# Kernel optimization log

Hardware: AMD Instinct MI355X
Metric: run time of the kernel (lower is better)

Reference implementation:

```python
import jax, jax.numpy as jnp
import numpy as np

T = 8192
C = 768
HEAD = 64

def setup_inputs() -> dict:
    key = jax.random.key(0)
    k0, k1, k2, k3 = jax.random.split(key, 4)
    tokens = jax.random.normal(k0, (T, C), dtype=jnp.float32)
    Wk = jax.random.normal(k1, (C, HEAD), dtype=jnp.float32) * (1.0 / np.sqrt(C))
    Wq = jax.random.normal(k2, (C, HEAD), dtype=jnp.float32) * (1.0 / np.sqrt(C))
    Wv = jax.random.normal(k3, (C, HEAD), dtype=jnp.float32) * (1.0 / np.sqrt(C))
    return {"tokens": tokens, "Wk": Wk, "Wq": Wq, "Wv": Wv}

def reference(tokens, Wk, Wq, Wv):
    # Single-head causal attention, faithful to source (scale = C**0.5, a multiply).
    keys = tokens @ Wk          # [T, H]
    queries = tokens @ Wq       # [T, H]
    values = tokens @ Wv        # [T, H]
    c = tokens.shape[-1]
    wei = (queries @ keys.T) * (c ** 0.5)                 # [T, T]
    causal = jnp.tril(jnp.ones((tokens.shape[0], tokens.shape[0]), dtype=bool))
    wei = jnp.where(causal, wei, -jnp.inf)
    wei = jax.nn.softmax(wei, axis=-1)
    return wei @ values         # [T, H]; dropout inactive (training=False)
```

## Files before the change

### kernel.cpp

```cpp
#include <hip/hip_runtime.h>
#include <math.h>

#define T_TOK 8192
#define C_DIM 768
#define H_DIM 64
#define SCALE_LOG2E (27.712812921102035f * 1.4426950408889634f)
#define NSPLIT 4

typedef _Float16 half8 __attribute__((ext_vector_type(8)));
typedef float floatx4 __attribute__((ext_vector_type(4)));

#define MFMA16(a, b, c) __builtin_amdgcn_mfma_f32_16x16x32_f16(a, b, c, 0, 0, 0)
#define WAIT_LGKM0() __builtin_amdgcn_s_waitcnt(0xC07F)
#define EXP2F(x) __builtin_amdgcn_exp2f(x)

typedef __attribute__((address_space(3))) void lds_void;
typedef const __attribute__((address_space(1))) void gbl_void;
#define GLOAD16(gp, lp) \
    __builtin_amdgcn_global_load_lds((gbl_void*)(gp), (lds_void*)(lp), 16, 0, 0)

template <int K> struct IC { static constexpr int v = K; };


__global__ __launch_bounds__(64) void wconvert_kernel(
    const float* __restrict__ Wk, const float* __restrict__ Wq,
    const float* __restrict__ Wv, _Float16* __restrict__ WF)
{
    const int b = blockIdx.x;
    const int mat = b / 96, rem = b % 96, kt = rem >> 2, nb = rem & 3;
    const int lane = threadIdx.x & 63, l15 = lane & 15, quad = lane >> 4;
    const float* __restrict__ W = (mat == 0) ? Wk : (mat == 1) ? Wq : Wv;

    half8 h, l;
#pragma unroll
    for (int j = 0; j < 8; ++j) {
        const float v = W[(kt * 32 + quad * 8 + j) * H_DIM + nb * 16 + l15];
        const _Float16 hv = (_Float16)v;
        h[j] = hv;
        l[j] = (_Float16)(v - (float)hv);
    }
    _Float16* dst = WF + ((((size_t)mat * 24 + kt) * 4 + nb) * 2) * 512 + lane * 8;
    *(half8*)dst = h;
    *(half8*)(dst + 512) = l;
}

__global__ __launch_bounds__(128, 1) void proj_kernel(
    const float* __restrict__ tokens, const _Float16* __restrict__ WF,
    _Float16* __restrict__ KF, _Float16* __restrict__ QF,
    _Float16* __restrict__ VF)
{
    __shared__ __align__(16) char smemraw[81920];
    const int b = blockIdx.x;
    const int tid = threadIdx.x;
    const int w = tid >> 6;
    const int lane = tid & 63, l15 = lane & 15, quad = lane >> 4;
    const int row0 = b * 32;
    const int kt0 = w * 12;

    floatx4 acc[3][2][4];
#pragma unroll
    for (int mat = 0; mat < 3; ++mat)
#pragma unroll
        for (int mb = 0; mb < 2; ++mb)
#pragma unroll
            for (int nb = 0; nb < 4; ++nb) acc[mat][mb][nb] = 0;

    const float* __restrict__ xb0 =
        tokens + (size_t)(row0 + l15) * C_DIM + kt0 * 32 + quad * 8;
    const float* __restrict__ xb1 =
        tokens + (size_t)(row0 + 16 + l15) * C_DIM + kt0 * 32 + quad * 8;

    _Float16* const wavebuf = (_Float16*)(smemraw + w * 40960);


    {
#pragma unroll
        for (int nb = 0; nb < 4; ++nb) {
            const _Float16* gK =
                WF + (size_t)((kt0 * 4 + nb) * 2) * 512 + lane * 8;
            const _Float16* gQ =
                WF + (size_t)(((24 + kt0) * 4 + nb) * 2) * 512 + lane * 8;
            const _Float16* gV =
                WF + (size_t)(((48 + kt0) * 4 + nb) * 2) * 512 + lane * 8;
            GLOAD16(gK,       wavebuf + (nb * 2 + 0) * 512);
            GLOAD16(gK + 512, wavebuf + (nb * 2 + 1) * 512);
            GLOAD16(gQ,       wavebuf + (8 + nb * 2 + 0) * 512);
            GLOAD16(gQ + 512, wavebuf + (8 + nb * 2 + 1) * 512);
            GLOAD16(gV,       wavebuf + (16 + nb) * 512);
        }
    }
    __builtin_amdgcn_sched_barrier(0);
    float4 tf[4][4];
#pragma unroll
    for (int d = 0; d < 4; ++d) {
        tf[d][0] = *(const float4*)(xb0 + d * 32);
        tf[d][1] = *(const float4*)(xb0 + d * 32 + 4);
        tf[d][2] = *(const float4*)(xb1 + d * 32);
        tf[d][3] = *(const float4*)(xb1 + d * 32 + 4);
    }
    __builtin_amdgcn_sched_barrier(0);

    auto iter = [&](auto kc) {
        constexpr int ktl = decltype(kc)::v;
        constexpr int slot = ktl & 3;
        constexpr int curb = ktl & 1;
        _Float16* wb  = wavebuf + curb * 10240;
        _Float16* wbn = wavebuf + (curb ^ 1) * 10240;

        __builtin_amdgcn_sched_barrier(0);
        const float4 x0 = tf[slot][0], x1 = tf[slot][1];
        const float4 x2 = tf[slot][2], x3 = tf[slot][3];
        __builtin_amdgcn_sched_barrier(0);

        if constexpr (ktl < 11) {
            const int ktn = kt0 + ktl + 1;
#pragma unroll
            for (int nb = 0; nb < 4; ++nb) {
                const _Float16* gK =
                    WF + (size_t)((ktn * 4 + nb) * 2) * 512 + lane * 8;
                const _Float16* gQ =
                    WF + (size_t)(((24 + ktn) * 4 + nb) * 2) * 512 + lane * 8;
                const _Float16* gV =
                    WF + (size_t)(((48 + ktn) * 4 + nb) * 2) * 512 + lane * 8;
                GLOAD16(gK,       wbn + (nb * 2 + 0) * 512);
                GLOAD16(gK + 512, wbn + (nb * 2 + 1) * 512);
                GLOAD16(gQ,       wbn + (8 + nb * 2 + 0) * 512);
                GLOAD16(gQ + 512, wbn + (8 + nb * 2 + 1) * 512);
                GLOAD16(gV,       wbn + (16 + nb) * 512);
            }
        }
        __builtin_amdgcn_sched_barrier(0);
        if constexpr (ktl + 4 < 12) {
            constexpr int ktf = ktl + 4;
            tf[slot][0] = *(const float4*)(xb0 + ktf * 32);
            tf[slot][1] = *(const float4*)(xb0 + ktf * 32 + 4);
            tf[slot][2] = *(const float4*)(xb1 + ktf * 32);
            tf[slot][3] = *(const float4*)(xb1 + ktf * 32 + 4);
        }
        __builtin_amdgcn_sched_barrier(0);
        constexpr int VMN = (ktl == 0)
            ? 40
            : ((ktl <= 8 ? 4 : 0) + (ktl <= 10 ? 20 : 0) + (ktl <= 7 ? 4 : 0));
        asm volatile("s_waitcnt vmcnt(%0)" ::"n"(VMN));
        __builtin_amdgcn_sched_barrier(0);

        half8 ah[2], al[2];
        {
            const float xs0[8] = {x0.x, x0.y, x0.z, x0.w, x1.x, x1.y, x1.z, x1.w};
            const float xs1[8] = {x2.x, x2.y, x2.z, x2.w, x3.x, x3.y, x3.z, x3.w};
#pragma unroll
            for (int e = 0; e < 8; ++e) {
                _Float16 hv = (_Float16)xs0[e];
                ah[0][e] = hv;
                al[0][e] = (_Float16)(xs0[e] - (float)hv);
                hv = (_Float16)xs1[e];
                ah[1][e] = hv;
                al[1][e] = (_Float16)(xs1[e] - (float)hv);
            }
        }
        const _Float16* wp = wb + lane * 8;
#pragma unroll
        for (int nb = 0; nb < 4; ++nb) {
            const half8 kh = *(const half8*)(wp + (nb * 2 + 0) * 512);
            const half8 kl = *(const half8*)(wp + (nb * 2 + 1) * 512);
            const half8 qh = *(const half8*)(wp + (8 + nb * 2 + 0) * 512);
            const half8 ql = *(const half8*)(wp + (8 + nb * 2 + 1) * 512);
            const half8 vh = *(const half8*)(wp + (16 + nb) * 512);
#pragma unroll
            for (int mb = 0; mb < 2; ++mb) {
                acc[0][mb][nb] = MFMA16(ah[mb], kh, acc[0][mb][nb]);
                acc[0][mb][nb] = MFMA16(ah[mb], kl, acc[0][mb][nb]);
                acc[0][mb][nb] = MFMA16(al[mb], kh, acc[0][mb][nb]);
                acc[1][mb][nb] = MFMA16(ah[mb], qh, acc[1][mb][nb]);
                acc[1][mb][nb] = MFMA16(ah[mb], ql, acc[1][mb][nb]);
                acc[1][mb][nb] = MFMA16(al[mb], qh, acc[1][mb][nb]);
                acc[2][mb][nb] = MFMA16(ah[mb], vh, acc[2][mb][nb]);
            }
        }
    };
#define PITER(k) iter(IC<k>{});
    PITER(0)  PITER(1)  PITER(2)  PITER(3)  PITER(4)  PITER(5)
    PITER(6)  PITER(7)  PITER(8)  PITER(9)  PITER(10) PITER(11)
#undef PITER

    __syncthreads();

    float* Cb0 = (float*)smemraw;
    float* Cb1 = (float*)(smemraw + 26112);
    float* Cbw = w ? Cb1 : Cb0;
#pragma unroll
    for (int mat = 0; mat < 3; ++mat)
#pragma unroll
        for (int mb = 0; mb < 2; ++mb)
#pragma unroll
            for (int nb = 0; nb < 4; ++nb)
#pragma unroll
                for (int r = 0; r < 4; ++r)
                    Cbw[mat * 2176 + (mb * 16 + quad * 4 + r) * 68 + nb * 16 + l15] =
                        acc[mat][mb][nb][r];
    __syncthreads();

    {
        const int nbL = w;
#pragma unroll
        for (int ks = 0; ks < 2; ++ks) {
            {
                const int off = (nbL * 16 + l15) * 68 + ks * 32 + quad * 8;
                const float4 a0 = *(const float4*)(Cb0 + off);
                const float4 a1 = *(const float4*)(Cb0 + off + 4);
                const float4 b0 = *(const float4*)(Cb1 + off);
                const float4 b1 = *(const float4*)(Cb1 + off + 4);
                const float cs[8] = {a0.x + b0.x, a0.y + b0.y, a0.z + b0.z,
                                     a0.w + b0.w, a1.x + b1.x, a1.y + b1.y,
                                     a1.z + b1.z, a1.w + b1.w};
                half8 h, l;
#pragma unroll
                for (int e = 0; e < 8; ++e) {
                    const _Float16 hv = (_Float16)cs[e];
                    h[e] = hv;
                    l[e] = (_Float16)(cs[e] - (float)hv);
                }
                const int t = b >> 1, nb = (b & 1) * 2 + nbL;
                _Float16* dst =
                    KF + (((size_t)(t * 4 + nb) * 2 + ks) * 2) * 512 + lane * 8;
                *(half8*)dst = h;
                *(half8*)(dst + 512) = l;
            }
            {
                const int off =
                    2176 + (nbL * 16 + l15) * 68 + ks * 32 + quad * 8;
                const float4 a0 = *(const float4*)(Cb0 + off);
                const float4 a1 = *(const float4*)(Cb0 + off + 4);
                const float4 b0 = *(const float4*)(Cb1 + off);
                const float4 b1 = *(const float4*)(Cb1 + off + 4);
                const float cs[8] = {a0.x + b0.x, a0.y + b0.y, a0.z + b0.z,
                                     a0.w + b0.w, a1.x + b1.x, a1.y + b1.y,
                                     a1.z + b1.z, a1.w + b1.w};
                half8 h, l;
#pragma unroll
                for (int e = 0; e < 8; ++e) {
                    const _Float16 hv = (_Float16)cs[e];
                    h[e] = hv;
                    l[e] = (_Float16)(cs[e] - (float)hv);
                }
                const int rb = b * 2 + nbL;
                _Float16* dst = QF + (((size_t)rb * 2 + ks) * 2) * 512 + lane * 8;
                *(half8*)dst = h;
                *(half8*)(dst + 512) = l;
            }
        }
    }

    {
        const int t = b >> 1, ks = b & 1;
#pragma unroll
        for (int nbi = 0; nbi < 2; ++nbi) {
            const int nb = w * 2 + nbi;
            half8 h;
#pragma unroll
            for (int j = 0; j < 8; ++j) {
                const int off = 2 * 2176 + (quad * 8 + j) * 68 + nb * 16 + l15;
                h[j] = (_Float16)(Cb0[off] + Cb1[off]);
            }
            *(half8*)(VF + ((size_t)(t * 4 + nb) * 2 + ks) * 512 + lane * 8) = h;
        }
    }
}

__global__ __launch_bounds__(512, 2) void attn_mfma_kernel(
    const _Float16* __restrict__ QF, const _Float16* __restrict__ KF,
    const _Float16* __restrict__ VF,
    float* __restrict__ pm, float* __restrict__ pl, float* __restrict__ po)
{
    __shared__ __align__(16) float smemf[9216];
    _Float16* Ps = (_Float16*)smemf;

    const int w = threadIdx.x >> 6, lane = threadIdx.x & 63;
    const int l15 = lane & 15, quad = lane >> 4;
    const int mhalf = w & 1, ss = w >> 1;

    const int b = blockIdx.x;
    const int j = b & 255, hb = b >> 8;
    const int qt = (hb == 0) ? (j >> 1) : (127 - (j >> 1));
    const int sp = (hb << 1) | (j & 1);

    const int qbase = qt * 64;
    const int wrow0 = qbase + mhalf * 32;

    half8 qh[2][2], ql[2][2];
#pragma unroll
    for (int mb = 0; mb < 2; ++mb)
#pragma unroll
        for (int ks = 0; ks < 2; ++ks) {
            const int rb = qt * 4 + mhalf * 2 + mb;
            const _Float16* qp = QF + (((size_t)rb * 2 + ks) * 2) * 512 + lane * 8;
            qh[mb][ks] = *(const half8*)qp;
            ql[mb][ks] = *(const half8*)(qp + 512);
        }

    floatx4 O[2][4];
#pragma unroll
    for (int mb = 0; mb < 2; ++mb)
#pragma unroll
        for (int nb = 0; nb < 4; ++nb) O[mb][nb] = 0;
    float mreg[2][4], lreg[2][4];
#pragma unroll
    for (int mb = 0; mb < 2; ++mb)
#pragma unroll
        for (int r = 0; r < 4; ++r) { mreg[mb][r] = -INFINITY; lreg[mb][r] = 0.f; }

    const int t0 = sp + 4 * ss;
    half8 bh[4][2], bl[4][2];
    if (t0 <= qt) {
#pragma unroll
        for (int nb = 0; nb < 4; ++nb)
#pragma unroll
            for (int ks = 0; ks < 2; ++ks) {
                const _Float16* kp =
                    KF + (((size_t)(t0 * 4 + nb) * 2 + ks) * 2) * 512 + lane * 8;
                bh[nb][ks] = *(const half8*)kp;
                bl[nb][ks] = *(const half8*)(kp + 512);
            }
    }

    for (int t = t0; t <= qt; t += 16) {
        const int kb = t * 64;

        half8 v0r[4], v1r[4];
#pragma unroll
        for (int nb = 0; nb < 4; ++nb) {
            const _Float16* vp = VF + ((size_t)(t * 4 + nb) * 2) * 512 + lane * 8;
            v0r[nb] = *(const half8*)vp;
            v1r[nb] = *(const half8*)(vp + 512);
        }

        float sv[2][4][4];
#pragma unroll
        for (int mb = 0; mb < 2; ++mb)
#pragma unroll
            for (int nb = 0; nb < 4; ++nb) {
                floatx4 s = 0;
#pragma unroll
                for (int ks = 0; ks < 2; ++ks) {
                    s = MFMA16(qh[mb][ks], bh[nb][ks], s);
                    s = MFMA16(qh[mb][ks], bl[nb][ks], s);
                    s = MFMA16(ql[mb][ks], bh[nb][ks], s);
                }
#pragma unroll
                for (int r = 0; r < 4; ++r) sv[mb][nb][r] = s[r] * SCALE_LOG2E;
            }

        if (t + 16 <= qt) {
            const int tn = t + 16;
#pragma unroll
            for (int nb = 0; nb < 4; ++nb)
#pragma unroll
                for (int ks = 0; ks < 2; ++ks) {
                    const _Float16* kp =
                        KF + (((size_t)(tn * 4 + nb) * 2 + ks) * 2) * 512 + lane * 8;
                    bh[nb][ks] = *(const half8*)kp;
                    bl[nb][ks] = *(const half8*)(kp + 512);
                }
        }

        if (kb + 63 > wrow0) {
#pragma unroll
            for (int mb = 0; mb < 2; ++mb) {
                const int rowbase = wrow0 + mb * 16 + quad * 4;
#pragma unroll
                for (int nb = 0; nb < 4; ++nb) {
                    const int col = kb + nb * 16 + l15;
#pragma unroll
                    for (int r = 0; r < 4; ++r)
                        if (col > rowbase + r) sv[mb][nb][r] = -INFINITY;
                }
            }
        }

#pragma unroll
        for (int mb = 0; mb < 2; ++mb) {
#pragma unroll
            for (int r = 0; r < 4; ++r) {
                float rm = fmaxf(fmaxf(sv[mb][0][r], sv[mb][1][r]),
                                 fmaxf(sv[mb][2][r], sv[mb][3][r]));
                rm = fmaxf(rm, __shfl_xor(rm, 1));
                rm = fmaxf(rm, __shfl_xor(rm, 2));
                rm = fmaxf(rm, __shfl_xor(rm, 4));
                rm = fmaxf(rm, __shfl_xor(rm, 8));
                const float mnew = fmaxf(mreg[mb][r], rm);
                const float alpha = EXP2F(mreg[mb][r] - mnew);
                float psum = 0.f;
#pragma unroll
                for (int nb = 0; nb < 4; ++nb) {
                    const float p = EXP2F(sv[mb][nb][r] - mnew);
                    psum += p;
                    Ps[(w * 2 + mb) * 1152 + (quad * 4 + r) * 72 + nb * 16 + l15] =
                        (_Float16)p;
                }
                lreg[mb][r] = lreg[mb][r] * alpha + psum;
                mreg[mb][r] = mnew;
#pragma unroll
                for (int nb = 0; nb < 4; ++nb) O[mb][nb][r] *= alpha;
            }
        }

        __builtin_amdgcn_wave_barrier();
        WAIT_LGKM0();
        __builtin_amdgcn_wave_barrier();
        half8 pa0[2], pa1[2];
#pragma unroll
        for (int mb = 0; mb < 2; ++mb) {
            const _Float16* pp = Ps + (w * 2 + mb) * 1152 + l15 * 72 + quad * 8;
            pa0[mb] = *(const half8*)pp;
            pa1[mb] = *(const half8*)(pp + 32);
        }

#pragma unroll
        for (int nb = 0; nb < 4; ++nb) {
#pragma unroll
            for (int mb = 0; mb < 2; ++mb) {
                O[mb][nb] = MFMA16(pa0[mb], v0r[nb], O[mb][nb]);
                O[mb][nb] = MFMA16(pa1[mb], v1r[nb], O[mb][nb]);
            }
        }
        __builtin_amdgcn_wave_barrier();
    }

#pragma unroll
    for (int mb = 0; mb < 2; ++mb)
#pragma unroll
        for (int r = 0; r < 4; ++r) {
            float s = lreg[mb][r];
            s += __shfl_xor(s, 1);
            s += __shfl_xor(s, 2);
            s += __shfl_xor(s, 4);
            s += __shfl_xor(s, 8);
            lreg[mb][r] = s;
        }

    __syncthreads();
    if (ss >= 2) {
        const int slot = ss - 2;
#pragma unroll
        for (int mb = 0; mb < 2; ++mb)
#pragma unroll
            for (int r = 0; r < 4; ++r) {
                const int row32 = mb * 16 + quad * 4 + r;
                const int sidx = (slot * 2 + mhalf) * 32 + row32;
#pragma unroll
                for (int nb = 0; nb < 4; ++nb)
                    smemf[sidx * 64 + nb * 16 + l15] = O[mb][nb][r];
                if (l15 == 0) {
                    smemf[8192 + sidx] = mreg[mb][r];
                    smemf[8320 + sidx] = lreg[mb][r];
                }
            }
    }
    __syncthreads();
    if (ss < 2) {
        const int slot = ss;
#pragma unroll
        for (int mb = 0; mb < 2; ++mb)
#pragma unroll
            for (int r = 0; r < 4; ++r) {
                const int row32 = mb * 16 + quad * 4 + r;
                const int sidx = (slot * 2 + mhalf) * 32 + row32;
                const float m1 = mreg[mb][r], l1 = lreg[mb][r];
                const float m2 = smemf[8192 + sidx];
                const float l2 = smemf[8320 + sidx];
                const float mm = fmaxf(m1, m2);
                const float a1 = (m1 == -INFINITY) ? 0.f : EXP2F(m1 - mm);
                const float a2 = (m2 == -INFINITY) ? 0.f : EXP2F(m2 - mm);
#pragma unroll
                for (int nb = 0; nb < 4; ++nb)
                    O[mb][nb][r] = O[mb][nb][r] * a1 +
                                   smemf[sidx * 64 + nb * 16 + l15] * a2;
                mreg[mb][r] = mm;
                lreg[mb][r] = l1 * a1 + l2 * a2;
            }
    }
    __syncthreads();
    if (ss == 1) {
#pragma unroll
        for (int mb = 0; mb < 2; ++mb)
#pragma unroll
            for (int r = 0; r < 4; ++r) {
                const int row32 = mb * 16 + quad * 4 + r;
                const int sidx = mhalf * 32 + row32;
#pragma unroll
                for (int nb = 0; nb < 4; ++nb)
                    smemf[sidx * 64 + nb * 16 + l15] = O[mb][nb][r];
                if (l15 == 0) {
                    smemf[8192 + sidx] = mreg[mb][r];
                    smemf[8320 + sidx] = lreg[mb][r];
                }
            }
    }
    __syncthreads();
    if (ss == 0) {
        const int pidx = qt * NSPLIT + sp;
#pragma unroll
        for (int mb = 0; mb < 2; ++mb)
#pragma unroll
            for (int r = 0; r < 4; ++r) {
                const int row32 = mb * 16 + quad * 4 + r;
                const int sidx = mhalf * 32 + row32;
                const float m1 = mreg[mb][r], l1 = lreg[mb][r];
                const float m2 = smemf[8192 + sidx];
                const float l2 = smemf[8320 + sidx];
                const float mm = fmaxf(m1, m2);
                const float a1 = (m1 == -INFINITY) ? 0.f : EXP2F(m1 - mm);
                const float a2 = (m2 == -INFINITY) ? 0.f : EXP2F(m2 - mm);
                const int row = mhalf * 32 + row32;
                float* dst = po + ((size_t)pidx * 64 + row) * 64;
#pragma unroll
                for (int nb = 0; nb < 4; ++nb)
                    dst[nb * 16 + l15] =
                        O[mb][nb][r] * a1 + smemf[sidx * 64 + nb * 16 + l15] * a2;
                if (l15 == 0) {
                    pm[pidx * 64 + row] = mm;
                    pl[pidx * 64 + row] = l1 * a1 + l2 * a2;
                }
            }
    }
}

__global__ __launch_bounds__(256) void combine_kernel(
    const float* __restrict__ pm, const float* __restrict__ pl,
    const float* __restrict__ po, float* __restrict__ out)
{
    const int vid = blockIdx.x * 256 + threadIdx.x;
    const int row = vid >> 4;
    const int d4  = vid & 15;
    const int qt  = row >> 6;
    const int r   = row & 63;

    float mm = -INFINITY;
#pragma unroll
    for (int s = 0; s < NSPLIT; ++s)
        mm = fmaxf(mm, pm[(qt * NSPLIT + s) * 64 + r]);
    float L = 0.f;
    float4 val = make_float4(0.f, 0.f, 0.f, 0.f);
#pragma unroll
    for (int s = 0; s < NSPLIT; ++s) {
        const int p = (qt * NSPLIT + s) * 64 + r;
        const float mp = pm[p];
        const float sc = (mp > -INFINITY) ? EXP2F(mp - mm) : 0.f;
        L += pl[p] * sc;
        const float4 v = *(const float4*)(po + (size_t)p * H_DIM + d4 * 4);
        val.x += v.x * sc; val.y += v.y * sc;
        val.z += v.z * sc; val.w += v.w * sc;
    }
    const float inv = 1.0f / L;
    float4 o; o.x = val.x * inv; o.y = val.y * inv;
    o.z = val.z * inv; o.w = val.w * inv;
    *(float4*)(out + (size_t)row * H_DIM + d4 * 4) = o;
}

extern "C" void kernel_launch(void* const* d_in, const int* in_sizes, int n_in,
                              void* d_out, int out_size, void* d_ws, size_t ws_size,
                              hipStream_t stream)
{
    const float* tokens = (const float*)d_in[0];
    const float* Wk = (const float*)d_in[1];
    const float* Wq = (const float*)d_in[2];
    const float* Wv = (const float*)d_in[3];
    float* out = (float*)d_out;

    char* ws = (char*)d_ws;
    const size_t MB = 1024 * 1024;
    _Float16* WF = (_Float16*)(ws + 0 * MB);
    _Float16* KF = (_Float16*)(ws + 1 * MB);
    _Float16* QF = (_Float16*)(ws + 3 * MB);
    _Float16* VF = (_Float16*)(ws + 5 * MB);
    float* pm = (float*)(ws + 6 * MB);
    float* pl = (float*)(ws + 6 * MB + 128 * 1024);
    float* po = (float*)(ws + 6 * MB + 256 * 1024);

    wconvert_kernel<<<288, 64, 0, stream>>>(Wk, Wq, Wv, WF);

    proj_kernel<<<256, 128, 0, stream>>>(tokens, WF, KF, QF, VF);

    attn_mfma_kernel<<<128 * NSPLIT, 512, 0, stream>>>(QF, KF, VF, pm, pl, po);

    combine_kernel<<<T_TOK * H_DIM / 4 / 256, 256, 0, stream>>>(pm, pl, po, out);
}
```

Measured before the change: 125.8 us.

## Compute transposed score tiles so softmax row reductions stay mostly in-lane

Swaps the MFMA operands so each score tile is K·Q^T. Each lane then holds 16 scores for one query row, so the row max needs two cross-lane shuffles instead of four per row-register. Because the row layout no longer matches the output accumulator, the per-row rescale factors and final m/l values pass through small LDS buffers, and P is packed with cvt_pkrtz into 8-byte LDS stores. This adds extra LDS traffic and shared memory per block, plus round-toward-zero rounding of P.

```diff
diff --git a/kernel.cpp b/kernel.cpp
--- a/kernel.cpp
+++ b/kernel.cpp
@@ -8,6 +8,7 @@
 #define NSPLIT 4
 
 typedef _Float16 half8 __attribute__((ext_vector_type(8)));
+typedef _Float16 half2t __attribute__((ext_vector_type(2)));
 typedef float floatx4 __attribute__((ext_vector_type(4)));
 
 #define MFMA16(a, b, c) __builtin_amdgcn_mfma_f32_16x16x32_f16(a, b, c, 0, 0, 0)
@@ -272,8 +273,11 @@
     const _Float16* __restrict__ VF,
     float* __restrict__ pm, float* __restrict__ pl, float* __restrict__ po)
 {
-    __shared__ __align__(16) float smemf[9216];
+    __shared__ __align__(16) float smemf[9984];
     _Float16* Ps = (_Float16*)smemf;
+    float* aL = smemf + 9216;
+    float* mP = smemf + 9472;
+    float* lP = smemf + 9728;
 
     const int w = threadIdx.x >> 6, lane = threadIdx.x & 63;
     const int l15 = lane & 15, quad = lane >> 4;
@@ -303,23 +307,20 @@
     for (int mb = 0; mb < 2; ++mb)
 #pragma unroll
         for (int nb = 0; nb < 4; ++nb) O[mb][nb] = 0;
-    float mreg[2][4], lreg[2][4];
-#pragma unroll
-    for (int mb = 0; mb < 2; ++mb)
-#pragma unroll
-        for (int r = 0; r < 4; ++r) { mreg[mb][r] = -INFINITY; lreg[mb][r] = 0.f; }
+    float mq[2] = {-INFINITY, -INFINITY};
+    float lq[2] = {0.f, 0.f};
 
     const int t0 = sp + 4 * ss;
-    half8 bh[4][2], bl[4][2];
+    half8 kh[4][2], kl[4][2];
     if (t0 <= qt) {
 #pragma unroll
-        for (int nb = 0; nb < 4; ++nb)
+        for (int kb2 = 0; kb2 < 4; ++kb2)
 #pragma unroll
             for (int ks = 0; ks < 2; ++ks) {
                 const _Float16* kp =
-                    KF + (((size_t)(t0 * 4 + nb) * 2 + ks) * 2) * 512 + lane * 8;
-                bh[nb][ks] = *(const half8*)kp;
-                bl[nb][ks] = *(const half8*)(kp + 512);
+                    KF + (((size_t)(t0 * 4 + kb2) * 2 + ks) * 2) * 512 + lane * 8;
+                kh[kb2][ks] = *(const half8*)kp;
+                kl[kb2][ks] = *(const half8*)(kp + 512);
             }
     }
 
@@ -334,79 +335,96 @@
             v1r[nb] = *(const half8*)(vp + 512);
         }
 
-        float sv[2][4][4];
-#pragma unroll
-        for (int mb = 0; mb < 2; ++mb)
-#pragma unroll
-            for (int nb = 0; nb < 4; ++nb) {
+        float sv[4][2][4];
+#pragma unroll
+        for (int kb2 = 0; kb2 < 4; ++kb2)
+#pragma unroll
+            for (int qb = 0; qb < 2; ++qb) {
                 floatx4 s = 0;
 #pragma unroll
                 for (int ks = 0; ks < 2; ++ks) {
-                    s = MFMA16(qh[mb][ks], bh[nb][ks], s);
-                    s = MFMA16(qh[mb][ks], bl[nb][ks], s);
-                    s = MFMA16(ql[mb][ks], bh[nb][ks], s);
-                }
-#pragma unroll
-                for (int r = 0; r < 4; ++r) sv[mb][nb][r] = s[r] * SCALE_LOG2E;
+                    s = MFMA16(kh[kb2][ks], qh[qb][ks], s);
+                    s = MFMA16(kl[kb2][ks], qh[qb][ks], s);
+                    s = MFMA16(kh[kb2][ks], ql[qb][ks], s);
+                }
+#pragma unroll
+                for (int r = 0; r < 4; ++r) sv[kb2][qb][r] = s[r] * SCALE_LOG2E;
             }
 
         if (t + 16 <= qt) {
             const int tn = t + 16;
 #pragma unroll
-            for (int nb = 0; nb < 4; ++nb)
+            for (int kb2 = 0; kb2 < 4; ++kb2)
 #pragma unroll
                 for (int ks = 0; ks < 2; ++ks) {
                     const _Float16* kp =
-                        KF + (((size_t)(tn * 4 + nb) * 2 + ks) * 2) * 512 + lane * 8;
-                    bh[nb][ks] = *(const half8*)kp;
-                    bl[nb][ks] = *(const half8*)(kp + 512);
+                        KF + (((size_t)(tn * 4 + kb2) * 2 + ks) * 2) * 512 + lane * 8;
+                    kh[kb2][ks] = *(const half8*)kp;
+                    kl[kb2][ks] = *(const half8*)(kp + 512);
                 }
         }
 
         if (kb + 63 > wrow0) {
 #pragma unroll
-            for (int mb = 0; mb < 2; ++mb) {
-                const int rowbase = wrow0 + mb * 16 + quad * 4;
-#pragma unroll
-                for (int nb = 0; nb < 4; ++nb) {
-                    const int col = kb + nb * 16 + l15;
+            for (int qb = 0; qb < 2; ++qb) {
+                const int q = wrow0 + qb * 16 + l15;
+#pragma unroll
+                for (int kb2 = 0; kb2 < 4; ++kb2) {
+                    const int keyb = kb + kb2 * 16 + quad * 4;
 #pragma unroll
                     for (int r = 0; r < 4; ++r)
-                        if (col > rowbase + r) sv[mb][nb][r] = -INFINITY;
-                }
-            }
-        }
-
-#pragma unroll
-        for (int mb = 0; mb < 2; ++mb) {
-#pragma unroll
-            for (int r = 0; r < 4; ++r) {
-                float rm = fmaxf(fmaxf(sv[mb][0][r], sv[mb][1][r]),
-                                 fmaxf(sv[mb][2][r], sv[mb][3][r]));
-                rm = fmaxf(rm, __shfl_xor(rm, 1));
-                rm = fmaxf(rm, __shfl_xor(rm, 2));
-                rm = fmaxf(rm, __shfl_xor(rm, 4));
-                rm = fmaxf(rm, __shfl_xor(rm, 8));
-                const float mnew = fmaxf(mreg[mb][r], rm);
-                const float alpha = EXP2F(mreg[mb][r] - mnew);
-                float psum = 0.f;
-#pragma unroll
-                for (int nb = 0; nb < 4; ++nb) {
-                    const float p = EXP2F(sv[mb][nb][r] - mnew);
-                    psum += p;
-                    Ps[(w * 2 + mb) * 1152 + (quad * 4 + r) * 72 + nb * 16 + l15] =
-                        (_Float16)p;
-                }
-                lreg[mb][r] = lreg[mb][r] * alpha + psum;
-                mreg[mb][r] = mnew;
-#pragma unroll
-                for (int nb = 0; nb < 4; ++nb) O[mb][nb][r] *= alpha;
-            }
+                        if (keyb + r > q) sv[kb2][qb][r] = -INFINITY;
+                }
+            }
+        }
+
+#pragma unroll
+        for (int qb = 0; qb < 2; ++qb) {
+            float rm = sv[0][qb][0];
+#pragma unroll
+            for (int kb2 = 0; kb2 < 4; ++kb2)
+#pragma unroll
+                for (int r = 0; r < 4; ++r) rm = fmaxf(rm, sv[kb2][qb][r]);
+            rm = fmaxf(rm, __shfl_xor(rm, 16));
+            rm = fmaxf(rm, __shfl_xor(rm, 32));
+            const float mnew = fmaxf(mq[qb], rm);
+            const float alpha = EXP2F(mq[qb] - mnew);
+            if (quad == 0) aL[w * 32 + qb * 16 + l15] = alpha;
+            float psum = 0.f;
+#pragma unroll
+            for (int kb2 = 0; kb2 < 4; ++kb2) {
+                const float p0 = EXP2F(sv[kb2][qb][0] - mnew);
+                const float p1 = EXP2F(sv[kb2][qb][1] - mnew);
+                const float p2 = EXP2F(sv[kb2][qb][2] - mnew);
+                const float p3 = EXP2F(sv[kb2][qb][3] - mnew);
+                psum += (p0 + p1) + (p2 + p3);
+                const unsigned u0 =
+                    __builtin_bit_cast(unsigned, __builtin_amdgcn_cvt_pkrtz(p0, p1));
+                const unsigned u1 =
+                    __builtin_bit_cast(unsigned, __builtin_amdgcn_cvt_pkrtz(p2, p3));
+                uint2* dst = (uint2*)(Ps + (w * 2 + qb) * 1152 + l15 * 72 +
+                                      kb2 * 16 + quad * 4);
+                *dst = make_uint2(u0, u1);
+            }
+            lq[qb] = lq[qb] * alpha + psum;
+            mq[qb] = mnew;
         }
 
         __builtin_amdgcn_wave_barrier();
         WAIT_LGKM0();
         __builtin_amdgcn_wave_barrier();
+
+        floatx4 aO[2];
+#pragma unroll
+        for (int mb = 0; mb < 2; ++mb)
+            aO[mb] = *(const floatx4*)(aL + w * 32 + mb * 16 + quad * 4);
+#pragma unroll
+        for (int mb = 0; mb < 2; ++mb)
+#pragma unroll
+            for (int nb = 0; nb < 4; ++nb)
+#pragma unroll
+                for (int r = 0; r < 4; ++r) O[mb][nb][r] *= aO[mb][r];
+
         half8 pa0[2], pa1[2];
 #pragma unroll
         for (int mb = 0; mb < 2; ++mb) {
@@ -427,16 +445,28 @@
     }
 
 #pragma unroll
-    for (int mb = 0; mb < 2; ++mb)
-#pragma unroll
-        for (int r = 0; r < 4; ++r) {
-            float s = lreg[mb][r];
-            s += __shfl_xor(s, 1);
-            s += __shfl_xor(s, 2);
-            s += __shfl_xor(s, 4);
-            s += __shfl_xor(s, 8);
-            lreg[mb][r] = s;
-        }
+    for (int qb = 0; qb < 2; ++qb) {
+        lq[qb] += __shfl_xor(lq[qb], 16);
+        lq[qb] += __shfl_xor(lq[qb], 32);
+    }
+    if (quad == 0) {
+#pragma unroll
+        for (int qb = 0; qb < 2; ++qb) {
+            mP[w * 32 + qb * 16 + l15] = mq[qb];
+            lP[w * 32 + qb * 16 + l15] = lq[qb];
+        }
+    }
+    __builtin_amdgcn_wave_barrier();
+    WAIT_LGKM0();
+    __builtin_amdgcn_wave_barrier();
+    float mreg[2][4], lreg[2][4];
+#pragma unroll
+    for (int mb = 0; mb < 2; ++mb) {
+        const floatx4 mv = *(const floatx4*)(mP + w * 32 + mb * 16 + quad * 4);
+        const floatx4 lv = *(const floatx4*)(lP + w * 32 + mb * 16 + quad * 4);
+#pragma unroll
+        for (int r = 0; r < 4; ++r) { mreg[mb][r] = mv[r]; lreg[mb][r] = lv[r]; }
+    }
 
     __syncthreads();
     if (ss >= 2) {
```

Result: faster. 117.0 us (-7.0%).
